# Optimization experiments

Measured on AMD Instinct MI355X. Metric: run time of the kernel, lower is better.

Reference implementation:

```python
import jax, jax.numpy as jnp
import numpy as np

INPUT_SIZE = 256
OUTPUT_SIZE = 128
N = 8192
SLOPE = 0.01
NEG_BIG = -9e15


def setup_inputs() -> dict:
    key = jax.random.key(0)
    k_h, k_adj, k_W, k_a = jax.random.split(key, 4)
    h = jax.random.normal(k_h, (N, INPUT_SIZE), dtype=jnp.float32)
    adj = jax.random.randint(k_adj, (N, N), 0, 2, dtype=jnp.int32)
    # xavier_uniform with gain=1.414
    gain = 1.414
    lim_W = gain * np.sqrt(6.0 / (INPUT_SIZE + OUTPUT_SIZE))
    W = jax.random.uniform(k_W, (INPUT_SIZE, OUTPUT_SIZE), dtype=jnp.float32, minval=-lim_W, maxval=lim_W)
    lim_a = gain * np.sqrt(6.0 / (2 * OUTPUT_SIZE + 1))
    a = jax.random.uniform(k_a, (2 * OUTPUT_SIZE, 1), dtype=jnp.float32, minval=-lim_a, maxval=lim_a)
    return {"h": h, "adj": adj, "W": W, "a": a}


def reference(h, adj, W, a):
    # Wh: [N, F]
    Wh = h @ W
    Fo = Wh.shape[1]
    # Original builds [N, N, 2F] concat then matmul with a; equivalent to
    # e[i, j] = leaky_relu(Wh[i] . a[:F] + Wh[j] . a[F:]) via broadcasting.
    src = Wh @ a[:Fo, 0]   # [N]
    dst = Wh @ a[Fo:, 0]   # [N]
    e = jax.nn.leaky_relu(src[:, None] + dst[None, :], negative_slope=SLOPE)  # [N, N]
    att = jnp.where(adj > 0, e, NEG_BIG)
    att = jax.nn.softmax(att, axis=1)
    return att @ Wh
```

## Files before the change

kernel.cpp:

```cpp
#include <hip/hip_runtime.h>
#include <hip/hip_bf16.h>

typedef unsigned short u16;
typedef unsigned int u32;
typedef __attribute__((ext_vector_type(8))) short short8;
typedef __attribute__((ext_vector_type(4))) float f32x4;

#define NN 8192
#define KIN 256
#define FOUT 128
#define SPLITS 8
#define KPER (NN / SPLITS)
#define KSTEPS (KPER / 32)
#define L2E 1.4426950408889634f

__device__ __forceinline__ float exp2fast(float x) { return __builtin_amdgcn_exp2f(x); }

__device__ __forceinline__ u16 f2bf(float f) {
    u32 u = __float_as_uint(f);
    u32 r = ((u >> 16) & 1u) + 0x7fffu;
    return (u16)((u + r) >> 16);
}
__device__ __forceinline__ u32 pk_bf16(float a, float b) {
    union { __hip_bfloat162 h2; u32 u; } cv;
    cv.h2 = __float22bfloat162_rn(make_float2(a, b));
    return cv.u;
}
__device__ __forceinline__ u32 fkey(float f) {
    u32 b = __float_as_uint(f);
    return (b & 0x80000000u) ? ~b : (b | 0x80000000u);
}
__device__ __forceinline__ float funkey(u32 k) {
    u32 b = (k & 0x80000000u) ? (k & 0x7fffffffu) : ~k;
    return __uint_as_float(b);
}

__global__ __launch_bounds__(512) void k1_wh(
    const float* __restrict__ h, const float* __restrict__ W, const float* __restrict__ a,
    u16* __restrict__ whfrag,
    float* __restrict__ src, float* __restrict__ dl2e, u32* __restrict__ gmaxk)
{
    __shared__ float hT[64][36];
    __shared__ u16   lt[128][40];
    __shared__ float sd[32][2];
    const int t  = threadIdx.x;
    const int m0 = blockIdx.x * 32;
    const int rq = t >> 5, cq = t & 31;

    float acc[2][4];
#pragma unroll
    for (int i = 0; i < 2; i++)
#pragma unroll
        for (int j = 0; j < 4; j++) acc[i][j] = 0.f;
    if (t < 64) sd[t >> 1][t & 1] = 0.f;

    for (int kt = 0; kt < KIN; kt += 64) {
        __syncthreads();
        {
            int r = t >> 4, kc = (t & 15) * 4;
            float4 hv = *(const float4*)(h + (size_t)(m0 + r) * KIN + kt + kc);
            hT[kc + 0][r] = hv.x; hT[kc + 1][r] = hv.y;
            hT[kc + 2][r] = hv.z; hT[kc + 3][r] = hv.w;
        }
        __syncthreads();
        for (int k = 0; k < 64; k++) {
            float4 wv = *(const float4*)(W + (size_t)(kt + k) * FOUT + cq * 4);
            float h0 = hT[k][rq * 2 + 0], h1 = hT[k][rq * 2 + 1];
            acc[0][0] += h0 * wv.x; acc[0][1] += h0 * wv.y; acc[0][2] += h0 * wv.z; acc[0][3] += h0 * wv.w;
            acc[1][0] += h1 * wv.x; acc[1][1] += h1 * wv.y; acc[1][2] += h1 * wv.z; acc[1][3] += h1 * wv.w;
        }
    }
#pragma unroll
    for (int i = 0; i < 2; i++) {
        int row = rq * 2 + i;
        float sp = 0.f, dp = 0.f;
#pragma unroll
        for (int j = 0; j < 4; j++) {
            sp += acc[i][j] * a[cq * 4 + j];
            dp += acc[i][j] * a[FOUT + cq * 4 + j];
            lt[cq * 4 + j][row] = f2bf(acc[i][j]);
        }
        atomicAdd(&sd[row][0], sp);
        atomicAdd(&sd[row][1], dp);
    }
    __syncthreads();
    if (t < 32) { src[m0 + t] = sd[t][0]; dl2e[m0 + t] = sd[t][1] * L2E; }
    if (t < 64) {
        float v = (t < 32) ? sd[t][1] : -3.0e38f;
#pragma unroll
        for (int off = 32; off >= 1; off >>= 1) v = fmaxf(v, __shfl_down(v, off));
        if (t == 0) atomicMax(gmaxk, fkey(v));
    }
    const int kstep = blockIdx.x;
    {
        int nt = t >> 6;
        int l  = t & 63;
        short8 v = *(const short8*)&lt[nt * 16 + (l & 15)][(l >> 4) * 8];
        *(short8*)(whfrag + ((size_t)(kstep * 8 + nt) * 64 + l) * 8) = v;
    }
}

__global__ __launch_bounds__(256, 2) void k2_attn(
    const int* __restrict__ adj, const float* __restrict__ src, const float* __restrict__ dl2e,
    const u16* __restrict__ whfrag, const u32* __restrict__ gmaxk,
    float* __restrict__ accp, float* __restrict__ lp)
{
    const int t = threadIdx.x;
    const int lane = t & 63, wave = t >> 6;
    const int strip2 = blockIdx.x * 4 + wave;
    const int i0 = strip2 * 32;
    const int split = blockIdx.y;
    const int l15 = lane & 15;
    const int kq = (lane >> 4) * 8;

    float sp0 = src[i0 + l15] * L2E;
    float sp1 = src[i0 + 16 + l15] * L2E;
    float gm = funkey(*gmaxk) * L2E;
    float x0 = sp0 + gm, x1 = sp1 + gm;
    float C0 = fmaxf(x0, 0.01f * x0), C1 = fmaxf(x1, 0.01f * x1);
    const float y1a = sp0 - C0, y2a = 0.01f * sp0 - C0;
    const float y1b = sp1 - C1, y2b = 0.01f * sp1 - C1;

    const int* arow0 = adj + (size_t)(i0 + l15) * NN;
    const int* arow1 = adj + (size_t)(i0 + 16 + l15) * NN;
    const int st0 = blockIdx.x & (KSTEPS - 1);
    const int kbase = split * KPER;

    f32x4 acc0[8], acc1[8];
#pragma unroll
    for (int nt = 0; nt < 8; nt++) { acc0[nt] = {0.f, 0.f, 0.f, 0.f}; acc1[nt] = {0.f, 0.f, 0.f, 0.f}; }
    float psum0 = 0.f, psum1 = 0.f;

    int4 a0L[2], a0H[2], a1L[2], a1H[2];
#pragma unroll
    for (int s = 0; s < 2; s++) {
        int kb = kbase + ((st0 + s) & (KSTEPS - 1)) * 32;
        a0L[s] = *(const int4*)(arow0 + kb + kq);
        a0H[s] = *(const int4*)(arow0 + kb + kq + 4);
        a1L[s] = *(const int4*)(arow1 + kb + kq);
        a1H[s] = *(const int4*)(arow1 + kb + kq + 4);
    }

#pragma unroll 4
    for (int it = 0; it < KSTEPS; ++it) {
        const int sl = it & 1;
        const int kb = kbase + ((st0 + it) & (KSTEPS - 1)) * 32;

        uint4 bv[8];
        const u16* wf = whfrag + ((size_t)(kb >> 5) * 8 * 64 + lane) * 8;
#pragma unroll
        for (int nt = 0; nt < 8; nt++)
            bv[nt] = *(const uint4*)(wf + (size_t)nt * 64 * 8);

        const float4 dl = *(const float4*)(dl2e + kb + kq);
        const float4 dh = *(const float4*)(dl2e + kb + kq + 4);

        int4 al = a0L[sl], ah = a0H[sl];
        float q0, q1, q2, q3, q4, q5, q6, q7;
        {
            float x;
            x = fmaxf(y1a + dl.x, y2a + 0.01f * dl.x); q0 = exp2fast(al.x > 0 ? x : -1.0e9f);
            x = fmaxf(y1a + dl.y, y2a + 0.01f * dl.y); q1 = exp2fast(al.y > 0 ? x : -1.0e9f);
            x = fmaxf(y1a + dl.z, y2a + 0.01f * dl.z); q2 = exp2fast(al.z > 0 ? x : -1.0e9f);
            x = fmaxf(y1a + dl.w, y2a + 0.01f * dl.w); q3 = exp2fast(al.w > 0 ? x : -1.0e9f);
            x = fmaxf(y1a + dh.x, y2a + 0.01f * dh.x); q4 = exp2fast(ah.x > 0 ? x : -1.0e9f);
            x = fmaxf(y1a + dh.y, y2a + 0.01f * dh.y); q5 = exp2fast(ah.y > 0 ? x : -1.0e9f);
            x = fmaxf(y1a + dh.z, y2a + 0.01f * dh.z); q6 = exp2fast(ah.z > 0 ? x : -1.0e9f);
            x = fmaxf(y1a + dh.w, y2a + 0.01f * dh.w); q7 = exp2fast(ah.w > 0 ? x : -1.0e9f);
        }
        psum0 += ((q0 + q1) + (q2 + q3)) + ((q4 + q5) + (q6 + q7));
        union { short8 s8; u32 u[4]; } af0;
        af0.u[0] = pk_bf16(q0, q1); af0.u[1] = pk_bf16(q2, q3);
        af0.u[2] = pk_bf16(q4, q5); af0.u[3] = pk_bf16(q6, q7);

        al = a1L[sl]; ah = a1H[sl];
        {
            float x;
            x = fmaxf(y1b + dl.x, y2b + 0.01f * dl.x); q0 = exp2fast(al.x > 0 ? x : -1.0e9f);
            x = fmaxf(y1b + dl.y, y2b + 0.01f * dl.y); q1 = exp2fast(al.y > 0 ? x : -1.0e9f);
            x = fmaxf(y1b + dl.z, y2b + 0.01f * dl.z); q2 = exp2fast(al.z > 0 ? x : -1.0e9f);
            x = fmaxf(y1b + dl.w, y2b + 0.01f * dl.w); q3 = exp2fast(al.w > 0 ? x : -1.0e9f);
            x = fmaxf(y1b + dh.x, y2b + 0.01f * dh.x); q4 = exp2fast(ah.x > 0 ? x : -1.0e9f);
            x = fmaxf(y1b + dh.y, y2b + 0.01f * dh.y); q5 = exp2fast(ah.y > 0 ? x : -1.0e9f);
            x = fmaxf(y1b + dh.z, y2b + 0.01f * dh.z); q6 = exp2fast(ah.z > 0 ? x : -1.0e9f);
            x = fmaxf(y1b + dh.w, y2b + 0.01f * dh.w); q7 = exp2fast(ah.w > 0 ? x : -1.0e9f);
        }
        psum1 += ((q0 + q1) + (q2 + q3)) + ((q4 + q5) + (q6 + q7));
        union { short8 s8; u32 u[4]; } af1;
        af1.u[0] = pk_bf16(q0, q1); af1.u[1] = pk_bf16(q2, q3);
        af1.u[2] = pk_bf16(q4, q5); af1.u[3] = pk_bf16(q6, q7);

        {
            int kb2 = kbase + ((st0 + it + 2) & (KSTEPS - 1)) * 32;
            a0L[sl] = *(const int4*)(arow0 + kb2 + kq);
            a0H[sl] = *(const int4*)(arow0 + kb2 + kq + 4);
            a1L[sl] = *(const int4*)(arow1 + kb2 + kq);
            a1H[sl] = *(const int4*)(arow1 + kb2 + kq + 4);
        }

#pragma unroll
        for (int nt = 0; nt < 8; nt++) {
            union { uint4 q; short8 s8; } bf; bf.q = bv[nt];
            acc0[nt] = __builtin_amdgcn_mfma_f32_16x16x32_bf16(af0.s8, bf.s8, acc0[nt], 0, 0, 0);
            acc1[nt] = __builtin_amdgcn_mfma_f32_16x16x32_bf16(af1.s8, bf.s8, acc1[nt], 0, 0, 0);
        }
    }

    float v0 = psum0;
    v0 += __shfl_down(v0, 32);
    v0 += __shfl_down(v0, 16);
    float v1 = psum1;
    v1 += __shfl_down(v1, 32);
    v1 += __shfl_down(v1, 16);
    if (lane < 16) {
        lp[split * NN + i0 + lane] = v0;
        lp[split * NN + i0 + 16 + lane] = v1;
    }

    float* ab2 = accp + (size_t)split * (NN * FOUT);
    const int s16a = strip2 * 2, s16b = strip2 * 2 + 1;
#pragma unroll
    for (int nt = 0; nt < 8; nt++)
        *(f32x4*)&ab2[((size_t)(s16a * 8 + nt) * 64 + lane) * 4] = acc0[nt];
#pragma unroll
    for (int nt = 0; nt < 8; nt++)
        *(f32x4*)&ab2[((size_t)(s16b * 8 + nt) * 64 + lane) * 4] = acc1[nt];
}

__global__ __launch_bounds__(256) void k2b_rsum(const float* __restrict__ lp,
                                               float* __restrict__ rinv)
{
    int i = blockIdx.x * 256 + threadIdx.x;
    float s = 0.f;
#pragma unroll
    for (int sp = 0; sp < SPLITS; sp++) s += lp[sp * NN + i];
    rinv[i] = 1.0f / s;
}

__global__ __launch_bounds__(256) void k3_comb(
    const float* __restrict__ accp, const float* __restrict__ rinv, float* __restrict__ out)
{
    int idx = blockIdx.x * 256 + threadIdx.x;
    int tile = idx >> 6, l = idx & 63;
    float4 s = make_float4(0.f, 0.f, 0.f, 0.f);
#pragma unroll
    for (int sp = 0; sp < SPLITS; sp++) {
        float4 v = *(const float4*)(accp + (size_t)sp * (NN * FOUT) + (size_t)idx * 4);
        s.x += v.x; s.y += v.y; s.z += v.z; s.w += v.w;
    }
    int row0 = (tile >> 3) * 16 + (l >> 4) * 4;
    int col  = (tile & 7) * 16 + (l & 15);
    float4 ri = *(const float4*)(rinv + row0);
    out[(size_t)(row0 + 0) * FOUT + col] = s.x * ri.x;
    out[(size_t)(row0 + 1) * FOUT + col] = s.y * ri.y;
    out[(size_t)(row0 + 2) * FOUT + col] = s.z * ri.z;
    out[(size_t)(row0 + 3) * FOUT + col] = s.w * ri.w;
}

extern "C" void kernel_launch(void* const* d_in, const int* in_sizes, int n_in,
                              void* d_out, int out_size, void* d_ws, size_t ws_size,
                              hipStream_t stream) {
    const float* h   = (const float*)d_in[0];
    const int*   adj = (const int*)d_in[1];
    const float* W   = (const float*)d_in[2];
    const float* a   = (const float*)d_in[3];
    float* out = (float*)d_out;

    char* ws = (char*)d_ws;
    u16*   whfrag = (u16*)ws;
    float* src    = (float*)(ws + (2u << 20));
    float* dl2e   = src + NN;
    u32*   gmaxk  = (u32*)(dl2e + NN);
    float* accp   = (float*)(ws + (3u << 20));
    float* lp     = (float*)(ws + (35u << 20));
    float* rinv   = (float*)(ws + (36u << 20));

    (void)hipMemsetAsync(gmaxk, 0, sizeof(u32), stream);
    k1_wh<<<dim3(NN / 32), dim3(512), 0, stream>>>(h, W, a, whfrag, src, dl2e, gmaxk);
    k2_attn<<<dim3(NN / 128, SPLITS), dim3(256), 0, stream>>>(adj, src, dl2e, whfrag, gmaxk, accp, lp);
    k2b_rsum<<<dim3(NN / 256), dim3(256), 0, stream>>>(lp, rinv);
    k3_comb<<<dim3((NN * FOUT / 4) / 256), dim3(256), 0, stream>>>(accp, rinv, out);
}
```

Before: 421.7 us.

## Load adjacency rows coalesced and compress to bitmasks via ballot

The attention kernel now reads each adjacency row in fully coalesced 256-int windows (each lane loads int4 of one row) instead of each lane gathering 8 scattered ints, then converts the mask to per-lane bitmask words using wave ballots. The destination logits for the split are staged once into shared memory rather than reloaded from global each step. Adjacency loads are software-pipelined across windows with double-buffered registers. This targets adjacency memory efficiency, which dominates the 256MB int32 read, at the cost of extra ballot/select ALU work and more register pressure.

```diff
diff --git a/kernel.cpp b/kernel.cpp
--- a/kernel.cpp
+++ b/kernel.cpp
@@ -3,6 +3,7 @@
 
 typedef unsigned short u16;
 typedef unsigned int u32;
+typedef unsigned long long u64;
 typedef __attribute__((ext_vector_type(8))) short short8;
 typedef __attribute__((ext_vector_type(4))) float f32x4;
 
@@ -105,13 +106,19 @@
     const u16* __restrict__ whfrag, const u32* __restrict__ gmaxk,
     float* __restrict__ accp, float* __restrict__ lp)
 {
+    __shared__ float4 sdl[KPER / 4];
     const int t = threadIdx.x;
     const int lane = t & 63, wave = t >> 6;
     const int strip2 = blockIdx.x * 4 + wave;
     const int i0 = strip2 * 32;
     const int split = blockIdx.y;
     const int l15 = lane & 15;
-    const int kq = (lane >> 4) * 8;
+    const int quad = lane >> 4;
+    const int q2 = quad * 2;
+    const int kbase = split * KPER;
+
+    sdl[t] = ((const float4*)(dl2e + kbase))[t];
+    __syncthreads();
 
     float sp0 = src[i0 + l15] * L2E;
     float sp1 = src[i0 + 16 + l15] * L2E;
@@ -121,90 +128,143 @@
     const float y1a = sp0 - C0, y2a = 0.01f * sp0 - C0;
     const float y1b = sp1 - C1, y2b = 0.01f * sp1 - C1;
 
-    const int* arow0 = adj + (size_t)(i0 + l15) * NN;
-    const int* arow1 = adj + (size_t)(i0 + 16 + l15) * NN;
-    const int st0 = blockIdx.x & (KSTEPS - 1);
-    const int kbase = split * KPER;
+    const int st0m = blockIdx.x & 3;
+    const int* abase = adj + (size_t)i0 * NN + kbase;
 
     f32x4 acc0[8], acc1[8];
 #pragma unroll
     for (int nt = 0; nt < 8; nt++) { acc0[nt] = {0.f, 0.f, 0.f, 0.f}; acc1[nt] = {0.f, 0.f, 0.f, 0.f}; }
     float psum0 = 0.f, psum1 = 0.f;
 
-    int4 a0L[2], a0H[2], a1L[2], a1H[2];
-#pragma unroll
-    for (int s = 0; s < 2; s++) {
-        int kb = kbase + ((st0 + s) & (KSTEPS - 1)) * 32;
-        a0L[s] = *(const int4*)(arow0 + kb + kq);
-        a0H[s] = *(const int4*)(arow0 + kb + kq + 4);
-        a1L[s] = *(const int4*)(arow1 + kb + kq);
-        a1H[s] = *(const int4*)(arow1 + kb + kq + 4);
-    }
-
-#pragma unroll 4
-    for (int it = 0; it < KSTEPS; ++it) {
-        const int sl = it & 1;
-        const int kb = kbase + ((st0 + it) & (KSTEPS - 1)) * 32;
-
-        uint4 bv[8];
-        const u16* wf = whfrag + ((size_t)(kb >> 5) * 8 * 64 + lane) * 8;
-#pragma unroll
-        for (int nt = 0; nt < 8; nt++)
-            bv[nt] = *(const uint4*)(wf + (size_t)nt * 64 * 8);
-
-        const float4 dl = *(const float4*)(dl2e + kb + kq);
-        const float4 dh = *(const float4*)(dl2e + kb + kq + 4);
-
-        int4 al = a0L[sl], ah = a0H[sl];
-        float q0, q1, q2, q3, q4, q5, q6, q7;
-        {
-            float x;
-            x = fmaxf(y1a + dl.x, y2a + 0.01f * dl.x); q0 = exp2fast(al.x > 0 ? x : -1.0e9f);
-            x = fmaxf(y1a + dl.y, y2a + 0.01f * dl.y); q1 = exp2fast(al.y > 0 ? x : -1.0e9f);
-            x = fmaxf(y1a + dl.z, y2a + 0.01f * dl.z); q2 = exp2fast(al.z > 0 ? x : -1.0e9f);
-            x = fmaxf(y1a + dl.w, y2a + 0.01f * dl.w); q3 = exp2fast(al.w > 0 ? x : -1.0e9f);
-            x = fmaxf(y1a + dh.x, y2a + 0.01f * dh.x); q4 = exp2fast(ah.x > 0 ? x : -1.0e9f);
-            x = fmaxf(y1a + dh.y, y2a + 0.01f * dh.y); q5 = exp2fast(ah.y > 0 ? x : -1.0e9f);
-            x = fmaxf(y1a + dh.z, y2a + 0.01f * dh.z); q6 = exp2fast(ah.z > 0 ? x : -1.0e9f);
-            x = fmaxf(y1a + dh.w, y2a + 0.01f * dh.w); q7 = exp2fast(ah.w > 0 ? x : -1.0e9f);
-        }
-        psum0 += ((q0 + q1) + (q2 + q3)) + ((q4 + q5) + (q6 + q7));
-        union { short8 s8; u32 u[4]; } af0;
-        af0.u[0] = pk_bf16(q0, q1); af0.u[1] = pk_bf16(q2, q3);
-        af0.u[2] = pk_bf16(q4, q5); af0.u[3] = pk_bf16(q6, q7);
-
-        al = a1L[sl]; ah = a1H[sl];
-        {
-            float x;
-            x = fmaxf(y1b + dl.x, y2b + 0.01f * dl.x); q0 = exp2fast(al.x > 0 ? x : -1.0e9f);
-            x = fmaxf(y1b + dl.y, y2b + 0.01f * dl.y); q1 = exp2fast(al.y > 0 ? x : -1.0e9f);
-            x = fmaxf(y1b + dl.z, y2b + 0.01f * dl.z); q2 = exp2fast(al.z > 0 ? x : -1.0e9f);
-            x = fmaxf(y1b + dl.w, y2b + 0.01f * dl.w); q3 = exp2fast(al.w > 0 ? x : -1.0e9f);
-            x = fmaxf(y1b + dh.x, y2b + 0.01f * dh.x); q4 = exp2fast(ah.x > 0 ? x : -1.0e9f);
-            x = fmaxf(y1b + dh.y, y2b + 0.01f * dh.y); q5 = exp2fast(ah.y > 0 ? x : -1.0e9f);
-            x = fmaxf(y1b + dh.z, y2b + 0.01f * dh.z); q6 = exp2fast(ah.z > 0 ? x : -1.0e9f);
-            x = fmaxf(y1b + dh.w, y2b + 0.01f * dh.w); q7 = exp2fast(ah.w > 0 ? x : -1.0e9f);
-        }
-        psum1 += ((q0 + q1) + (q2 + q3)) + ((q4 + q5) + (q6 + q7));
-        union { short8 s8; u32 u[4]; } af1;
-        af1.u[0] = pk_bf16(q0, q1); af1.u[1] = pk_bf16(q2, q3);
-        af1.u[2] = pk_bf16(q4, q5); af1.u[3] = pk_bf16(q6, q7);
-
-        {
-            int kb2 = kbase + ((st0 + it + 2) & (KSTEPS - 1)) * 32;
-            a0L[sl] = *(const int4*)(arow0 + kb2 + kq);
-            a0H[sl] = *(const int4*)(arow0 + kb2 + kq + 4);
-            a1L[sl] = *(const int4*)(arow1 + kb2 + kq);
-            a1H[sl] = *(const int4*)(arow1 + kb2 + kq + 4);
-        }
-
-#pragma unroll
-        for (int nt = 0; nt < 8; nt++) {
-            union { uint4 q; short8 s8; } bf; bf.q = bv[nt];
-            acc0[nt] = __builtin_amdgcn_mfma_f32_16x16x32_bf16(af0.s8, bf.s8, acc0[nt], 0, 0, 0);
-            acc1[nt] = __builtin_amdgcn_mfma_f32_16x16x32_bf16(af1.s8, bf.s8, acc1[nt], 0, 0, 0);
-        }
-    }
+    u32 w0lo[4], w0hi[4], w1lo[4], w1hi[4];
+    u32 n0lo[4], n0hi[4], n1lo[4], n1hi[4];
+    int4 rb[2][4];
+
+#define LOADB(s, r0, wdw) do { \
+    const int* ap_ = abase + (wdw) * 256 + lane * 4; \
+    rb[s][0] = *(const int4*)(ap_ + (size_t)((r0) + 0) * NN); \
+    rb[s][1] = *(const int4*)(ap_ + (size_t)((r0) + 1) * NN); \
+    rb[s][2] = *(const int4*)(ap_ + (size_t)((r0) + 2) * NN); \
+    rb[s][3] = *(const int4*)(ap_ + (size_t)((r0) + 3) * NN); \
+} while (0)
+
+#define BALLOT4(s, r0, TLO, THI, LB) do { \
+    _Pragma("unroll") \
+    for (int k_ = 0; k_ < 4; ++k_) { \
+        u64 b0_ = __ballot(rb[s][k_].x > 0); \
+        u64 b1_ = __ballot(rb[s][k_].y > 0); \
+        u64 b2_ = __ballot(rb[s][k_].z > 0); \
+        u64 b3_ = __ballot(rb[s][k_].w > 0); \
+        bool c_ = (l15 == ((r0) + k_) - (LB)); \
+        TLO[0] = c_ ? (u32)b0_ : TLO[0];  THI[0] = c_ ? (u32)(b0_ >> 32) : THI[0]; \
+        TLO[1] = c_ ? (u32)b1_ : TLO[1];  THI[1] = c_ ? (u32)(b1_ >> 32) : THI[1]; \
+        TLO[2] = c_ ? (u32)b2_ : TLO[2];  THI[2] = c_ ? (u32)(b2_ >> 32) : THI[2]; \
+        TLO[3] = c_ ? (u32)b3_ : TLO[3];  THI[3] = c_ ? (u32)(b3_ >> 32) : THI[3]; \
+    } \
+} while (0)
+
+#pragma unroll
+    for (int j = 0; j < 4; ++j) {
+        w0lo[j] = 0; w0hi[j] = 0; w1lo[j] = 0; w1hi[j] = 0;
+        n0lo[j] = 0; n0hi[j] = 0; n1lo[j] = 0; n1hi[j] = 0;
+    }
+
+    LOADB(0, 0, st0m);
+    LOADB(1, 4, st0m);
+    BALLOT4(0, 0,  w0lo, w0hi, 0);  LOADB(0, 8,  st0m);
+    BALLOT4(1, 4,  w0lo, w0hi, 0);  LOADB(1, 12, st0m);
+    BALLOT4(0, 8,  w0lo, w0hi, 0);  LOADB(0, 16, st0m);
+    BALLOT4(1, 12, w0lo, w0hi, 0);  LOADB(1, 20, st0m);
+    BALLOT4(0, 16, w1lo, w1hi, 16); LOADB(0, 24, st0m);
+    BALLOT4(1, 20, w1lo, w1hi, 16); LOADB(1, 28, st0m);
+    BALLOT4(0, 24, w1lo, w1hi, 16);
+    BALLOT4(1, 28, w1lo, w1hi, 16);
+    {
+        const int w1d = (st0m + 1) & 3;
+        LOADB(0, 0, w1d);
+        LOADB(1, 4, w1d);
+    }
+
+    for (int ss = 0; ss < 4; ++ss) {
+        const int wdwC = (st0m + ss) & 3;
+        const size_t wfss = (size_t)((kbase >> 5) + wdwC * 8) * 4096;
+#pragma unroll
+        for (int u = 0; u < 8; ++u) {
+            const int s = u & 1;
+
+            if (ss < 3) {
+                if (u < 4) { BALLOT4(s, 4 * u, n0lo, n0hi, 0); }
+                else       { BALLOT4(s, 4 * u, n1lo, n1hi, 16); }
+            }
+
+            uint4 bv[8];
+            const u16* wf = whfrag + wfss + (size_t)u * 4096 + lane * 8;
+#pragma unroll
+            for (int nt = 0; nt < 8; nt++)
+                bv[nt] = *(const uint4*)(wf + (size_t)nt * 512);
+
+            if (ss * 8 + u < 22) {
+                const int wdwI = (st0m + ((u < 6) ? ss + 1 : ss + 2)) & 3;
+                LOADB(s, 4 * ((u + 2) & 7), wdwI);
+            }
+
+            const float4 dl = sdl[wdwC * 64 + u * 8 + q2];
+            const float4 dh = sdl[wdwC * 64 + u * 8 + q2 + 1];
+
+            const int sh = ((u & 3) * 8) + q2;
+            u32 t0, t1, t2, t3, g0, g1, g2, g3;
+            if (u < 4) {
+                t0 = w0lo[0] >> sh; t1 = w0lo[1] >> sh; t2 = w0lo[2] >> sh; t3 = w0lo[3] >> sh;
+                g0 = w1lo[0] >> sh; g1 = w1lo[1] >> sh; g2 = w1lo[2] >> sh; g3 = w1lo[3] >> sh;
+            } else {
+                t0 = w0hi[0] >> sh; t1 = w0hi[1] >> sh; t2 = w0hi[2] >> sh; t3 = w0hi[3] >> sh;
+                g0 = w1hi[0] >> sh; g1 = w1hi[1] >> sh; g2 = w1hi[2] >> sh; g3 = w1hi[3] >> sh;
+            }
+
+            float x, q0, q1, q2_, q3, q4, q5, q6, q7;
+            x = fmaxf(y1a + dl.x, y2a + 0.01f * dl.x); q0  = exp2fast((t0 & 1u) ? x : -1.0e9f);
+            x = fmaxf(y1a + dl.y, y2a + 0.01f * dl.y); q1  = exp2fast((t1 & 1u) ? x : -1.0e9f);
+            x = fmaxf(y1a + dl.z, y2a + 0.01f * dl.z); q2_ = exp2fast((t2 & 1u) ? x : -1.0e9f);
+            x = fmaxf(y1a + dl.w, y2a + 0.01f * dl.w); q3  = exp2fast((t3 & 1u) ? x : -1.0e9f);
+            x = fmaxf(y1a + dh.x, y2a + 0.01f * dh.x); q4  = exp2fast((t0 & 2u) ? x : -1.0e9f);
+            x = fmaxf(y1a + dh.y, y2a + 0.01f * dh.y); q5  = exp2fast((t1 & 2u) ? x : -1.0e9f);
+            x = fmaxf(y1a + dh.z, y2a + 0.01f * dh.z); q6  = exp2fast((t2 & 2u) ? x : -1.0e9f);
+            x = fmaxf(y1a + dh.w, y2a + 0.01f * dh.w); q7  = exp2fast((t3 & 2u) ? x : -1.0e9f);
+            psum0 += ((q0 + q1) + (q2_ + q3)) + ((q4 + q5) + (q6 + q7));
+            union { short8 s8; u32 u4[4]; } af0;
+            af0.u4[0] = pk_bf16(q0, q1); af0.u4[1] = pk_bf16(q2_, q3);
+            af0.u4[2] = pk_bf16(q4, q5); af0.u4[3] = pk_bf16(q6, q7);
+
+            x = fmaxf(y1b + dl.x, y2b + 0.01f * dl.x); q0  = exp2fast((g0 & 1u) ? x : -1.0e9f);
+            x = fmaxf(y1b + dl.y, y2b + 0.01f * dl.y); q1  = exp2fast((g1 & 1u) ? x : -1.0e9f);
+            x = fmaxf(y1b + dl.z, y2b + 0.01f * dl.z); q2_ = exp2fast((g2 & 1u) ? x : -1.0e9f);
+            x = fmaxf(y1b + dl.w, y2b + 0.01f * dl.w); q3  = exp2fast((g3 & 1u) ? x : -1.0e9f);
+            x = fmaxf(y1b + dh.x, y2b + 0.01f * dh.x); q4  = exp2fast((g0 & 2u) ? x : -1.0e9f);
+            x = fmaxf(y1b + dh.y, y2b + 0.01f * dh.y); q5  = exp2fast((g1 & 2u) ? x : -1.0e9f);
+            x = fmaxf(y1b + dh.z, y2b + 0.01f * dh.z); q6  = exp2fast((g2 & 2u) ? x : -1.0e9f);
+            x = fmaxf(y1b + dh.w, y2b + 0.01f * dh.w); q7  = exp2fast((g3 & 2u) ? x : -1.0e9f);
+            psum1 += ((q0 + q1) + (q2_ + q3)) + ((q4 + q5) + (q6 + q7));
+            union { short8 s8; u32 u4[4]; } af1;
+            af1.u4[0] = pk_bf16(q0, q1); af1.u4[1] = pk_bf16(q2_, q3);
+            af1.u4[2] = pk_bf16(q4, q5); af1.u4[3] = pk_bf16(q6, q7);
+
+#pragma unroll
+            for (int nt = 0; nt < 8; nt++) {
+                union { uint4 q; short8 s8; } bf; bf.q = bv[nt];
+                acc0[nt] = __builtin_amdgcn_mfma_f32_16x16x32_bf16(af0.s8, bf.s8, acc0[nt], 0, 0, 0);
+                acc1[nt] = __builtin_amdgcn_mfma_f32_16x16x32_bf16(af1.s8, bf.s8, acc1[nt], 0, 0, 0);
+            }
+        }
+        if (ss < 3) {
+#pragma unroll
+            for (int j = 0; j < 4; ++j) {
+                w0lo[j] = n0lo[j]; w0hi[j] = n0hi[j];
+                w1lo[j] = n1lo[j]; w1hi[j] = n1hi[j];
+            }
+        }
+    }
+#undef LOADB
+#undef BALLOT4
 
     float v0 = psum0;
     v0 += __shfl_down(v0, 32);
```

Result: slower. 449.0 us (+6.5%).
